# Kernel tuning notes

Hardware: AMD Instinct MI355X
Metric: run time of the kernel (lower is better)

## Reference

```python
import jax, jax.numpy as jnp
import numpy as np

EMB_DIM = 4096
OUT_DIM = 4096
T_PREV = 8192


def setup_inputs() -> dict:
    key = jax.random.key(0)
    ks = jax.random.split(key, 6)
    return {
        "x": jax.random.normal(ks[0], (1, EMB_DIM), dtype=jnp.float32),
        "W_query": jax.random.normal(ks[1], (OUT_DIM, EMB_DIM), dtype=jnp.float32) * 0.02,
        "W_key": jax.random.normal(ks[2], (OUT_DIM, EMB_DIM), dtype=jnp.float32) * 0.02,
        "W_value": jax.random.normal(ks[3], (OUT_DIM, EMB_DIM), dtype=jnp.float32) * 0.02,
        "K_cache": jax.random.normal(ks[4], (OUT_DIM, T_PREV), dtype=jnp.float32),
        "V_cache": jax.random.normal(ks[5], (OUT_DIM, T_PREV), dtype=jnp.float32),
    }


def reference(x, W_query, W_key, W_value, K_cache, V_cache):
    # x: [1, E] -> xt: [E, 1]
    xt = x.T
    q = W_query @ xt  # [D, 1]
    k = W_key @ xt    # [D, 1]
    v = W_value @ xt  # [D, 1]
    # append current step to caches (hstack semantics)
    K = jnp.concatenate([K_cache, k], axis=1)  # [D, T+1]
    V = jnp.concatenate([V_cache, v], axis=1)  # [D, T+1]
    # sigmoid-scored attention (NOT softmax)
    a = (q.reshape(1, -1) @ K) / jnp.sqrt(jnp.float32(OUT_DIM))  # [1, T+1]
    a = jax.nn.sigmoid(a)
    z = V @ a.reshape(-1, 1)  # [D, 1]
    return z
```

## Files before the change

### kernel.cpp

```cpp
#include <hip/hip_runtime.h>
#include <math.h>

#define EMB   4096
#define DIM   4096
#define TPREV 8192
#define TTOT  8193

#define WS_Q        0
#define WS_K        DIM
#define WS_V        (2*DIM)
#define WS_A        (3*DIM)
#define WS_PART     20544
#define NCHUNK      128
#define CHUNK_ROWS  32

__global__ __launch_bounds__(256) void qkv_kernel(
    const float* __restrict__ x,
    const float* __restrict__ Wq, const float* __restrict__ Wk,
    const float* __restrict__ Wv, float* __restrict__ ws) {
    int wave = threadIdx.x >> 6;
    int lane = threadIdx.x & 63;
    int g = blockIdx.x * 4 + wave;
    int m = g >> 12;
    int r = g & 4095;
    const float* W = (m == 0) ? Wq : (m == 1) ? Wk : Wv;

    const float4* row = (const float4*)(W + (size_t)r * EMB);
    const float4* xv  = (const float4*)x;

    float acc = 0.0f;
#pragma unroll 8
    for (int i = 0; i < EMB / 256; ++i) {
        float4 a = row[i * 64 + lane];
        float4 b = xv[i * 64 + lane];
        acc += a.x * b.x + a.y * b.y + a.z * b.z + a.w * b.w;
    }
#pragma unroll
    for (int off = 32; off > 0; off >>= 1) acc += __shfl_down(acc, off, 64);
    if (lane == 0) ws[m * DIM + r] = acc;
}

__global__ __launch_bounds__(256) void score_kernel(
    const float* __restrict__ Kc, float* __restrict__ ws) {
    const float* q = ws + WS_Q;
    float* part    = ws + WS_PART;

    __shared__ float qs[CHUNK_ROWS];
    int d0 = blockIdx.y * CHUNK_ROWS;
    if (threadIdx.x < CHUNK_ROWS) qs[threadIdx.x] = q[d0 + threadIdx.x];
    __syncthreads();

    int t = blockIdx.x * 1024 + threadIdx.x * 4;
    float4 acc = {0.f, 0.f, 0.f, 0.f};
#pragma unroll 8
    for (int i = 0; i < CHUNK_ROWS; ++i) {
        const float4 kv = *(const float4*)(Kc + (size_t)(d0 + i) * TPREV + t);
        float qd = qs[i];
        acc.x += qd * kv.x;
        acc.y += qd * kv.y;
        acc.z += qd * kv.z;
        acc.w += qd * kv.w;
    }
    *(float4*)(part + (size_t)blockIdx.y * TPREV + t) = acc;
}

__global__ __launch_bounds__(256) void reduce_sigmoid_kernel(
    float* __restrict__ ws) {
    float* scores      = ws + WS_A;
    const float* part  = ws + WS_PART;

    if (blockIdx.x < 32) {
        int t = blockIdx.x * 256 + threadIdx.x;
        float s = 0.0f;
#pragma unroll 16
        for (int c = 0; c < NCHUNK; ++c) s += part[(size_t)c * TPREV + t];
        s *= 0.015625f;
        scores[t] = 1.0f / (1.0f + __expf(-s));
    } else {
        const float* q = ws + WS_Q;
        const float* k = ws + WS_K;
        float s = 0.0f;
        int base = threadIdx.x * 16;
#pragma unroll 16
        for (int i = 0; i < 16; ++i) s += q[base + i] * k[base + i];
        __shared__ float red[256];
        red[threadIdx.x] = s;
        __syncthreads();
        for (int off = 128; off > 0; off >>= 1) {
            if (threadIdx.x < off) red[threadIdx.x] += red[threadIdx.x + off];
            __syncthreads();
        }
        if (threadIdx.x == 0) {
            float v = red[0] * 0.015625f;
            scores[TPREV] = 1.0f / (1.0f + __expf(-v));
        }
    }
}

__global__ __launch_bounds__(256) void out_kernel(
    const float* __restrict__ Vc, const float* __restrict__ ws,
    float* __restrict__ out) {
    const float* vvec = ws + WS_V;
    const float* a    = ws + WS_A;

    int wave = threadIdx.x >> 6;
    int lane = threadIdx.x & 63;
    int d = blockIdx.x * 4 + wave;

    const float4* row = (const float4*)(Vc + (size_t)d * TPREV);
    const float4* av  = (const float4*)a;

    float acc = 0.0f;
#pragma unroll 8
    for (int i = 0; i < TPREV / 256; ++i) {
        float4 vv = row[i * 64 + lane];
        float4 aa = av[i * 64 + lane];
        acc += vv.x * aa.x + vv.y * aa.y + vv.z * aa.z + vv.w * aa.w;
    }
#pragma unroll
    for (int off = 32; off > 0; off >>= 1) acc += __shfl_down(acc, off, 64);
    if (lane == 0) out[d] = acc + vvec[d] * a[TPREV];
}

extern "C" void kernel_launch(void* const* d_in, const int* in_sizes, int n_in,
                              void* d_out, int out_size, void* d_ws, size_t ws_size,
                              hipStream_t stream) {
    const float* x  = (const float*)d_in[0];
    const float* Wq = (const float*)d_in[1];
    const float* Wk = (const float*)d_in[2];
    const float* Wv = (const float*)d_in[3];
    const float* Kc = (const float*)d_in[4];
    const float* Vc = (const float*)d_in[5];
    float* out = (float*)d_out;
    float* ws  = (float*)d_ws;

    qkv_kernel<<<3072, 256, 0, stream>>>(x, Wq, Wk, Wv, ws);
    score_kernel<<<dim3(8, 128), 256, 0, stream>>>(Kc, ws);
    reduce_sigmoid_kernel<<<33, 256, 0, stream>>>(ws);
    out_kernel<<<1024, 256, 0, stream>>>(Vc, ws, out);
}
```

Measured before the change: 399.5 us.

## Use one block per row in GEMV kernels and parallelize partial reduction

The QKV and output GEMV kernels switch from one wave per row to one 256-thread block per row, loading all operands up front and combining wave partial sums through shared memory. The score kernel loads four K rows per step to expose more independent memory loads. The partial-sum reduction is split across 64 blocks, each using eight row slices and float4 loads, so the 128-way sum is spread over more threads. This aims for more loads in flight on memory-bound passes, at the cost of four times as many blocks plus an extra barrier per block.

```diff
diff --git a/kernel.cpp b/kernel.cpp
--- a/kernel.cpp
+++ b/kernel.cpp
@@ -14,30 +14,40 @@
 #define NCHUNK      128
 #define CHUNK_ROWS  32
 
+__device__ __forceinline__ float dot4(float4 a, float4 b) {
+    return a.x * b.x + a.y * b.y + a.z * b.z + a.w * b.w;
+}
+
 __global__ __launch_bounds__(256) void qkv_kernel(
     const float* __restrict__ x,
     const float* __restrict__ Wq, const float* __restrict__ Wk,
     const float* __restrict__ Wv, float* __restrict__ ws) {
-    int wave = threadIdx.x >> 6;
-    int lane = threadIdx.x & 63;
-    int g = blockIdx.x * 4 + wave;
-    int m = g >> 12;
-    int r = g & 4095;
+    int b = blockIdx.x;
+    int m = b >> 12;
+    int r = b & 4095;
     const float* W = (m == 0) ? Wq : (m == 1) ? Wk : Wv;
-
     const float4* row = (const float4*)(W + (size_t)r * EMB);
     const float4* xv  = (const float4*)x;
+    int tid = threadIdx.x;
 
-    float acc = 0.0f;
-#pragma unroll 8
-    for (int i = 0; i < EMB / 256; ++i) {
-        float4 a = row[i * 64 + lane];
-        float4 b = xv[i * 64 + lane];
-        acc += a.x * b.x + a.y * b.y + a.z * b.z + a.w * b.w;
-    }
+    float4 w0 = row[tid];
+    float4 w1 = row[tid + 256];
+    float4 w2 = row[tid + 512];
+    float4 w3 = row[tid + 768];
+    float4 x0 = xv[tid];
+    float4 x1 = xv[tid + 256];
+    float4 x2 = xv[tid + 512];
+    float4 x3 = xv[tid + 768];
+
+    float s = dot4(w0, x0) + dot4(w1, x1) + dot4(w2, x2) + dot4(w3, x3);
+
 #pragma unroll
-    for (int off = 32; off > 0; off >>= 1) acc += __shfl_down(acc, off, 64);
-    if (lane == 0) ws[m * DIM + r] = acc;
+    for (int off = 32; off > 0; off >>= 1) s += __shfl_down(s, off, 64);
+
+    __shared__ float red[4];
+    if ((tid & 63) == 0) red[tid >> 6] = s;
+    __syncthreads();
+    if (tid == 0) ws[m * DIM + r] = red[0] + red[1] + red[2] + red[3];
 }
 
 __global__ __launch_bounds__(256) void score_kernel(
@@ -50,32 +60,55 @@
     if (threadIdx.x < CHUNK_ROWS) qs[threadIdx.x] = q[d0 + threadIdx.x];
     __syncthreads();
 
-    int t = blockIdx.x * 1024 + threadIdx.x * 4;
+    size_t t = (size_t)blockIdx.x * 1024 + threadIdx.x * 4;
+    const float* base = Kc + (size_t)d0 * TPREV + t;
+
     float4 acc = {0.f, 0.f, 0.f, 0.f};
-#pragma unroll 8
-    for (int i = 0; i < CHUNK_ROWS; ++i) {
-        const float4 kv = *(const float4*)(Kc + (size_t)(d0 + i) * TPREV + t);
-        float qd = qs[i];
-        acc.x += qd * kv.x;
-        acc.y += qd * kv.y;
-        acc.z += qd * kv.z;
-        acc.w += qd * kv.w;
+#pragma unroll
+    for (int g = 0; g < CHUNK_ROWS / 4; ++g) {
+        float4 k0 = *(const float4*)(base + (size_t)(4 * g + 0) * TPREV);
+        float4 k1 = *(const float4*)(base + (size_t)(4 * g + 1) * TPREV);
+        float4 k2 = *(const float4*)(base + (size_t)(4 * g + 2) * TPREV);
+        float4 k3 = *(const float4*)(base + (size_t)(4 * g + 3) * TPREV);
+        float q0 = qs[4 * g], q1 = qs[4 * g + 1], q2 = qs[4 * g + 2], q3 = qs[4 * g + 3];
+        acc.x += q0 * k0.x + q1 * k1.x + q2 * k2.x + q3 * k3.x;
+        acc.y += q0 * k0.y + q1 * k1.y + q2 * k2.y + q3 * k3.y;
+        acc.z += q0 * k0.z + q1 * k1.z + q2 * k2.z + q3 * k3.z;
+        acc.w += q0 * k0.w + q1 * k1.w + q2 * k2.w + q3 * k3.w;
     }
     *(float4*)(part + (size_t)blockIdx.y * TPREV + t) = acc;
 }
 
 __global__ __launch_bounds__(256) void reduce_sigmoid_kernel(
     float* __restrict__ ws) {
-    float* scores      = ws + WS_A;
-    const float* part  = ws + WS_PART;
+    if (blockIdx.x < 64) {
+        const float4* p = (const float4*)(ws + WS_PART);
+        int f4    = threadIdx.x & 31;
+        int slice = threadIdx.x >> 5;
+        size_t idx = (size_t)(slice * 16) * (TPREV / 4) + (size_t)blockIdx.x * 32 + f4;
 
-    if (blockIdx.x < 32) {
-        int t = blockIdx.x * 256 + threadIdx.x;
-        float s = 0.0f;
-#pragma unroll 16
-        for (int c = 0; c < NCHUNK; ++c) s += part[(size_t)c * TPREV + t];
-        s *= 0.015625f;
-        scores[t] = 1.0f / (1.0f + __expf(-s));
+        float4 s = {0.f, 0.f, 0.f, 0.f};
+#pragma unroll 4
+        for (int c = 0; c < 16; ++c) {
+            float4 v = p[idx + (size_t)c * (TPREV / 4)];
+            s.x += v.x; s.y += v.y; s.z += v.z; s.w += v.w;
+        }
+        __shared__ float4 red[256];
+        red[threadIdx.x] = s;
+        __syncthreads();
+        if (threadIdx.x < 32) {
+            float4 tot = red[threadIdx.x];
+#pragma unroll
+            for (int sl = 1; sl < 8; ++sl) {
+                float4 v = red[sl * 32 + threadIdx.x];
+                tot.x += v.x; tot.y += v.y; tot.z += v.z; tot.w += v.w;
+            }
+            tot.x = 1.0f / (1.0f + __expf(-tot.x * 0.015625f));
+            tot.y = 1.0f / (1.0f + __expf(-tot.y * 0.015625f));
+            tot.z = 1.0f / (1.0f + __expf(-tot.z * 0.015625f));
+            tot.w = 1.0f / (1.0f + __expf(-tot.w * 0.015625f));
+            ((float4*)(ws + WS_A))[(size_t)blockIdx.x * 32 + threadIdx.x] = tot;
+        }
     } else {
         const float* q = ws + WS_Q;
         const float* k = ws + WS_K;
@@ -92,7 +125,7 @@
         }
         if (threadIdx.x == 0) {
             float v = red[0] * 0.015625f;
-            scores[TPREV] = 1.0f / (1.0f + __expf(-v));
+            ws[WS_A + TPREV] = 1.0f / (1.0f + __expf(-v));
         }
     }
 }
@@ -100,26 +133,35 @@
 __global__ __launch_bounds__(256) void out_kernel(
     const float* __restrict__ Vc, const float* __restrict__ ws,
     float* __restrict__ out) {
-    const float* vvec = ws + WS_V;
-    const float* a    = ws + WS_A;
+    int d = blockIdx.x;
+    const float4* row = (const float4*)(Vc + (size_t)d * TPREV);
+    const float4* av  = (const float4*)(ws + WS_A);
+    int tid = threadIdx.x;
 
-    int wave = threadIdx.x >> 6;
-    int lane = threadIdx.x & 63;
-    int d = blockIdx.x * 4 + wave;
+    float s = 0.0f;
+#pragma unroll
+    for (int g = 0; g < 2; ++g) {
+        int o = g * 1024;
+        float4 v0 = row[o + tid];
+        float4 v1 = row[o + tid + 256];
+        float4 v2 = row[o + tid + 512];
+        float4 v3 = row[o + tid + 768];
+        float4 a0 = av[o + tid];
+        float4 a1 = av[o + tid + 256];
+        float4 a2 = av[o + tid + 512];
+        float4 a3 = av[o + tid + 768];
+        s += dot4(v0, a0) + dot4(v1, a1) + dot4(v2, a2) + dot4(v3, a3);
+    }
 
-    const float4* row = (const float4*)(Vc + (size_t)d * TPREV);
-    const float4* av  = (const float4*)a;
+#pragma unroll
+    for (int off = 32; off > 0; off >>= 1) s += __shfl_down(s, off, 64);
 
-    float acc = 0.0f;
-#pragma unroll 8
-    for (int i = 0; i < TPREV / 256; ++i) {
-        float4 vv = row[i * 64 + lane];
-        float4 aa = av[i * 64 + lane];
-        acc += vv.x * aa.x + vv.y * aa.y + vv.z * aa.z + vv.w * aa.w;
-    }
-#pragma unroll
-    for (int off = 32; off > 0; off >>= 1) acc += __shfl_down(acc, off, 64);
-    if (lane == 0) out[d] = acc + vvec[d] * a[TPREV];
+    __shared__ float red[4];
+    if ((tid & 63) == 0) red[tid >> 6] = s;
+    __syncthreads();
+    if (tid == 0)
+        out[d] = red[0] + red[1] + red[2] + red[3]
+               + ws[WS_V + d] * ws[WS_A + TPREV];
 }
 
 extern "C" void kernel_launch(void* const* d_in, const int* in_sizes, int n_in,
@@ -134,8 +176,8 @@
     float* out = (float*)d_out;
     float* ws  = (float*)d_ws;
 
-    qkv_kernel<<<3072, 256, 0, stream>>>(x, Wq, Wk, Wv, ws);
+    qkv_kernel<<<12288, 256, 0, stream>>>(x, Wq, Wk, Wv, ws);
     score_kernel<<<dim3(8, 128), 256, 0, stream>>>(Kc, ws);
-    reduce_sigmoid_kernel<<<33, 256, 0, stream>>>(ws);
-    out_kernel<<<1024, 256, 0, stream>>>(Vc, ws, out);
+    reduce_sigmoid_kernel<<<65, 256, 0, stream>>>(ws);
+    out_kernel<<<4096, 256, 0, stream>>>(Vc, ws, out);
 }
```

Result: faster. 389.9 us (-2.4%).
